# Performance work log

Measured on AMD Instinct MI355X. Metric: run time of the kernel, lower is better.

## Reference

```python
import jax, jax.numpy as jnp
import numpy as np

K = 5                      # spline kernel_size per dim
NEG = -1e30                # finite -inf stand-in for max-scatter init
_COMBO = np.indices((2, 2, 2)).reshape(3, 8).T   # [8,3] corner offsets of the deg-1 B-spline support
_STRIDE = np.array([1, K, K * K])


def spline_basis(pseudo):
    # pseudo: [E,3] in [0,1]; open degree-1 B-spline, kernel_size K per dim.
    v = jnp.clip(pseudo, 0.0, 1.0) * (K - 1)
    i0 = jnp.clip(jnp.floor(v), 0, K - 2)
    f = v - i0                                   # [E,3] fractional part
    c = jnp.asarray(_COMBO)                      # [8,3]
    w = jnp.prod(jnp.where(c[None] == 1, f[:, None, :], 1.0 - f[:, None, :]), axis=2)  # [E,8]
    k = jnp.sum((i0.astype(jnp.int32)[:, None, :] + c[None]) * jnp.asarray(_STRIDE)[None, None, :], axis=2)  # [E,8]
    return w, k


def spline_conv(x, src, dst, pseudo, W, root, bias):
    # x:[N,Fin], W:[K^3,Fin,Fout]. Gather-spline-scatter, mean aggregation + root weight + bias.
    N = x.shape[0]
    U = jnp.einsum('ni,kio->nko', x, W)          # [N,K^3,Fout] all-kernel transform (dense GEMM)
    bw, kidx = spline_basis(pseudo)              # [E,8], [E,8]
    msg = jnp.sum(bw[:, :, None] * U[src[:, None], kidx], axis=1)  # [E,Fout]
    deg = jnp.zeros((N,), x.dtype).at[dst].add(1.0)
    agg = jnp.zeros((N, W.shape[2]), x.dtype).at[dst].add(msg) / jnp.maximum(deg, 1.0)[:, None]
    return agg + x @ root + bias


def weighted_max_pool(x, w, cluster, C):
    # keep features of the max-attention-weight node in each voxel cluster
    seg_w = jnp.full((C,), NEG, x.dtype).at[cluster].max(w)
    winner = w >= seg_w[cluster]
    pooled = jnp.full((C, x.shape[1]), NEG, x.dtype).at[cluster].max(jnp.where(winner[:, None], x, NEG))
    return jnp.where(pooled <= NEG / 2, 0.0, pooled)


def dense_max_pool(x, cluster, C):
    pooled = jnp.full((C, x.shape[1]), NEG, x.dtype).at[cluster].max(x)
    return jnp.where(pooled <= NEG / 2, 0.0, pooled)


def setup_inputs() -> dict:
    key = jax.random.key(0)
    ks = iter(jax.random.split(key, 80))
    N = [30000, 10000, 4000, 1500, 600]
    E = [360000, 120000, 48000, 18000, 7200]
    Fin = [1, 32, 64, 64, 64]
    Fout = [32, 64, 64, 64, 64]
    Cs = [10000, 4000, 1500, 600, 128]
    d = {"x": jax.random.normal(next(ks), (N[0], 1), jnp.float32)}
    for l in range(5):
        d[f"src{l}"] = jax.random.randint(next(ks), (E[l],), 0, N[l], jnp.int32)
        d[f"dst{l}"] = jax.random.randint(next(ks), (E[l],), 0, N[l], jnp.int32)
        d[f"pseudo{l}"] = jax.random.uniform(next(ks), (E[l], 3), jnp.float32)
    for l in range(5):
        d[f"cluster{l+1}"] = jax.random.randint(next(ks), (N[l],), 0, Cs[l], jnp.int32)
    for l in range(5):
        d[f"W{l+1}"] = 0.1 * jax.random.normal(next(ks), (K ** 3, Fin[l], Fout[l]), jnp.float32)
        d[f"root{l+1}"] = 0.1 * jax.random.normal(next(ks), (Fin[l], Fout[l]), jnp.float32)
        d[f"b{l+1}"] = jnp.zeros((Fout[l],), jnp.float32)
    for l, fdim in enumerate([32, 64, 64, 64]):
        d[f"attw{l+1}"] = 0.1 * jax.random.normal(next(ks), (fdim, 2), jnp.float32)
        d[f"attb{l+1}"] = jnp.zeros((2,), jnp.float32)
    d["fcw"] = 0.05 * jax.random.normal(next(ks), (512, 10), jnp.float32)
    d["fcb"] = jnp.zeros((10,), jnp.float32)
    return d


def reference(x, src0, dst0, pseudo0, src1, dst1, pseudo1, src2, dst2, pseudo2,
              src3, dst3, pseudo3, src4, dst4, pseudo4,
              cluster1, cluster2, cluster3, cluster4, cluster5,
              W1, root1, b1, W2, root2, b2, W3, root3, b3, W4, root4, b4, W5, root5, b5,
              attw1, attb1, attw2, attb2, attw3, attb3, attw4, attb4, fcw, fcb):
    h = jax.nn.elu(spline_conv(x, src0, dst0, pseudo0, W1, root1, b1))
    h = weighted_max_pool(h, (h @ attw1 + attb1)[:, 0], cluster1, 10000)
    h = jax.nn.elu(spline_conv(h, src1, dst1, pseudo1, W2, root2, b2))
    h = weighted_max_pool(h, (h @ attw2 + attb2)[:, 0], cluster2, 4000)
    h = jax.nn.elu(spline_conv(h, src2, dst2, pseudo2, W3, root3, b3))
    h = weighted_max_pool(h, (h @ attw3 + attb3)[:, 0], cluster3, 1500)
    h = jax.nn.elu(spline_conv(h, src3, dst3, pseudo3, W4, root4, b4))
    h = weighted_max_pool(h, (h @ attw4 + attb4)[:, 0], cluster4, 600)
    h = jax.nn.relu(spline_conv(h, src4, dst4, pseudo4, W5, root5, b5))
    h = dense_max_pool(h, cluster5, 128)        # [128, 64] = 16 graphs x 8 voxels
    z = h.reshape(-1, 512)                      # [16, 8*64]
    return jax.nn.log_softmax(z @ fcw + fcb, axis=1)
```

## Files before the change

kernel.cpp:

```cpp
#include <hip/hip_runtime.h>
#include <math.h>

#define KS 5

typedef __bf16 bf16x8 __attribute__((ext_vector_type(8)));
typedef float f32x4 __attribute__((ext_vector_type(4)));
typedef unsigned long long u64;

__device__ __forceinline__ unsigned int flipf(float f) {
    unsigned int b = __float_as_uint(f);
    return b ^ ((b >> 31) ? 0xFFFFFFFFu : 0x80000000u);
}
__device__ __forceinline__ float unflipf(unsigned int u) {
    unsigned int b = u ^ ((u >> 31) ? 0x80000000u : 0xFFFFFFFFu);
    return __uint_as_float(b);
}
__device__ __forceinline__ float pread(unsigned int u) {
    return (u == 0u) ? 0.f : unflipf(u);
}

__device__ __forceinline__ void basis1(float p, int& b, float& f) {
    float v = fminf(fmaxf(p, 0.f), 1.f) * (float)(KS - 1);
    float fl = fminf(floorf(v), (float)(KS - 2));
    b = (int)fl; f = v - fl;
}

__device__ const int cE[5]     = {360000, 120000, 48000, 18000, 7200};
__device__ const int cN[5]     = {30000, 10000, 4000, 1500, 600};
__device__ const int cNB[5]    = {512, 469, 188, 71, 29};
__device__ const int cStart[5] = {0, 512, 981, 1169, 1240};
__device__ const int cBTend[5] = {8192, 139264, 401408, 663552, 925696};
__device__ const int cLFIN[5]  = {0, 5, 6, 6, 6};
__device__ const int cLFOUT[5] = {5, 6, 6, 6, 6};
__device__ const int cLKB[5]   = {2, 5, 6, 6, 6};

#define PREP_BLOCKS 1269
#define BPACK_TOT   925696

struct BatchPtrs {
    const float* ps[5];
    const int*   dst[5];
    int*   cell[5];
    int*   ctrl[5];
    int*   blkbase[5];
    float* deg[5];
    float* rankf[5];
    int*   dstbase[5];
    int*   eord[5];
};

struct BpackPtrs {
    const float* W[5];
    __bf16* H[5];
    __bf16* M[5];
    __bf16* L[5];
};

__global__ void edge_prep_all(BatchPtrs P)
{
    __shared__ int lh[64];
    int b = blockIdx.x;
    int l = (b >= 512) + (b >= 981) + (b >= 1169) + (b >= 1240);
    int lb = b - cStart[l];
    int E = cE[l];
    int stride = cNB[l] * 256;
    const float* pseudo = P.ps[l];
    const int* dst = P.dst[l];
    int* cell = P.cell[l];
    float* deg = P.deg[l];
    float* rankf = P.rankf[l];

    int t = threadIdx.x;
    if (t < 64) lh[t] = 0;
    __syncthreads();
    for (int e = lb * 256 + t; e < E; e += stride) {
        int b0, b1, b2; float f0, f1, f2;
        basis1(pseudo[e * 3 + 0], b0, f0);
        basis1(pseudo[e * 3 + 1], b1, f1);
        basis1(pseudo[e * 3 + 2], b2, f2);
        int c = b0 + 4 * b1 + 16 * b2;
        cell[e] = c;
        atomicAdd(&lh[c], 1);
        rankf[e] = atomicAdd(&deg[dst[e]], 1.0f);
    }
    __syncthreads();
    if (t < 64) P.blkbase[l][lb * 64 + t] = atomicAdd(&P.ctrl[l][t], lh[t]);
}

__global__ void scan5(BatchPtrs P)
{
    __shared__ int wexc[16];
    __shared__ int tot;
    __shared__ int carry;
    int l = blockIdx.x;
    int* ctrl = P.ctrl[l];
    const float* deg = P.deg[l];
    int* dstbase = P.dstbase[l];
    int N = cN[l];

    int t = (int)threadIdx.x;
    int lane = t & 63;
    int wid = t >> 6;
    if (t == 0) carry = 0;
    if (t < 64) {
        int h = ctrl[t];
        int x = h;
        #pragma unroll
        for (int off = 1; off < 64; off <<= 1) {
            int y = __shfl_up(x, off, 64);
            if (lane >= off) x += y;
        }
        int excl = x - h;
        ctrl[128 + t] = excl;
        int ch = (h + 63) >> 6;
        int cx = ch;
        #pragma unroll
        for (int off = 1; off < 64; off <<= 1) {
            int y = __shfl_up(cx, off, 64);
            if (lane >= off) cx += y;
        }
        ctrl[200 + t] = cx - ch;
        if (t == 63) {
            ctrl[128 + 64] = excl + h;
            ctrl[200 + 64] = cx;
            ctrl[272] = cx;
        }
    }
    __syncthreads();
    for (int base = 0; base < N; base += 4096) {
        int i0 = base + t * 4;
        int4 v = make_int4(0, 0, 0, 0);
        if (i0 < N) {
            float4 d = *reinterpret_cast<const float4*>(deg + i0);
            v.x = (int)d.x; v.y = (int)d.y; v.z = (int)d.z; v.w = (int)d.w;
        }
        int s = v.x + v.y + v.z + v.w;
        int x = s;
        #pragma unroll
        for (int off = 1; off < 64; off <<= 1) {
            int y = __shfl_up(x, off, 64);
            if (lane >= off) x += y;
        }
        if (lane == 63) wexc[wid] = x;
        __syncthreads();
        if (t < 16) {
            int a = wexc[t];
            int inc = a;
            #pragma unroll
            for (int off = 1; off < 16; off <<= 1) {
                int y = __shfl_up(inc, off, 16);
                if (t >= off) inc += y;
            }
            wexc[t] = inc - a;
            if (t == 15) tot = inc;
        }
        __syncthreads();
        if (i0 < N) {
            int e0 = carry + wexc[wid] + (x - s);
            int4 o;
            o.x = e0;
            o.y = e0 + v.x;
            o.z = o.y + v.y;
            o.w = o.z + v.z;
            *reinterpret_cast<int4*>(dstbase + i0) = o;
        }
        __syncthreads();
        if (t == 0) carry += tot;
        __syncthreads();
    }
    if (t == 0) dstbase[N] = carry;
}

__global__ void edge_scatter_all(BatchPtrs P)
{
    __shared__ int cur[64];
    int b = blockIdx.x;
    int l = (b >= 512) + (b >= 981) + (b >= 1169) + (b >= 1240);
    int lb = b - cStart[l];
    int E = cE[l];
    int stride = cNB[l] * 256;
    const int* cell = P.cell[l];
    const int* dst = P.dst[l];
    const int* dstbase = P.dstbase[l];
    float* rankf = P.rankf[l];
    int* posb = (int*)rankf;
    int* eord = P.eord[l];

    int t = threadIdx.x;
    if (t < 64) cur[t] = P.ctrl[l][128 + t] + P.blkbase[l][lb * 64 + t];
    __syncthreads();
    for (int e = lb * 256 + t; e < E; e += stride) {
        int p = atomicAdd(&cur[cell[e]], 1);
        eord[p] = e;
        int r = (int)rankf[e];
        posb[e] = dstbase[dst[e]] + r;
    }
}

__global__ void bpack_all(BpackPtrs B)
{
    int t = blockIdx.x * blockDim.x + threadIdx.x;
    if (t >= BPACK_TOT) return;
    int l = (t >= 8192) + (t >= 139264) + (t >= 401408) + (t >= 663552);
    int tl = t - (l ? cBTend[l - 1] : 0);
    int lfout = cLFOUT[l], lkb = cLKB[l], lfin = cLFIN[l];
    int fin = 1 << lfin;
    const float* W = B.W[l];
    int o = tl & ((1 << lfout) - 1);
    int kb = (tl >> lfout) & ((1 << lkb) - 1);
    int cellid = tl >> (lfout + lkb);
    int b0 = cellid & 3, b1 = (cellid >> 2) & 3, b2 = cellid >> 4;
    bf16x8 vh, vm, vl;
    #pragma unroll
    for (int j = 0; j < 8; ++j) {
        int r = kb * 8 + j;
        float val = 0.f;
        if (r < (fin << 3)) {
            int c = r >> lfin;
            int i = r & (fin - 1);
            int k = (b0 + (c & 1)) + 5 * (b1 + ((c >> 1) & 1)) + 25 * (b2 + (c >> 2));
            val = W[((((size_t)k << lfin) + i) << lfout) + o];
        }
        __bf16 hv = (__bf16)val;
        vh[j] = hv;
        float r1 = val - (float)hv;
        __bf16 mv = (__bf16)r1;
        vm[j] = mv;
        vl[j] = (__bf16)(r1 - (float)mv);
    }
    *reinterpret_cast<bf16x8*>(B.H[l] + (size_t)tl * 8) = vh;
    *reinterpret_cast<bf16x8*>(B.M[l] + (size_t)tl * 8) = vm;
    *reinterpret_cast<bf16x8*>(B.L[l] + (size_t)tl * 8) = vl;
}

template<int FIN, int FOUT, bool GATHER>
__global__ void conv_mfma(const float* __restrict__ xin,
                          const u64* __restrict__ win,
                          const int* __restrict__ src,
                          const float* __restrict__ pseudo,
                          const __bf16* __restrict__ BpH,
                          const __bf16* __restrict__ BpM,
                          const __bf16* __restrict__ BpL,
                          const int* __restrict__ ctrl,
                          const int* __restrict__ eord,
                          const int* __restrict__ posb,
                          float* __restrict__ msg)
{
    constexpr int KB = (FIN == 1) ? 4 : FIN;
    constexpr int KSTEPS = (FIN == 1) ? 1 : FIN / 4;
    constexpr int NF = FOUT / 16;
    constexpr int SLICE = 4 * FOUT * 8;

    __shared__ float cst[64][FOUT + 1];
    __shared__ int posv[64];
    __shared__ __bf16 bsh[3][SLICE];

    int bid = blockIdx.x;
    if (bid >= ctrl[272]) return;
    int blo = 0, bhi = 64;
    while (blo + 1 < bhi) {
        int mid = (blo + bhi) >> 1;
        if (ctrl[200 + mid] <= bid) blo = mid; else bhi = mid;
    }
    int bucket = blo;
    int m0 = (bid - ctrl[200 + bucket]) << 6;
    int bbase = ctrl[128 + bucket];
    int bsize = ctrl[128 + bucket + 1] - bbase;

    int tt = threadIdx.x;
    int lane = tt & 63;
    int wave = tt >> 6;
    int h4 = lane >> 4;
    int col = lane & 15;
    int row = m0 + wave * 16 + col;
    bool valid = row < bsize;
    int e = eord[bbase + (valid ? row : 0)];
    int s = src[e];

    if (tt < 64) {
        int orow = m0 + tt;
        posv[tt] = (orow < bsize) ? posb[eord[bbase + orow]] : -1;
    }

    float bw[8];
    {
        int b0, b1, b2; float f0, f1, f2;
        basis1(pseudo[e * 3 + 0], b0, f0);
        basis1(pseudo[e * 3 + 1], b1, f1);
        basis1(pseudo[e * 3 + 2], b2, f2);
        float g0 = 1.f - f0, g1 = 1.f - f1, g2 = 1.f - f2;
        float vf = valid ? 1.f : 0.f;
        #pragma unroll
        for (int j = 0; j < 8; ++j)
            bw[j] = vf * ((j & 1) ? f0 : g0) * (((j >> 1) & 1) ? f1 : g1) * (((j >> 2) & 1) ? f2 : g2);
    }

    const float* xrow;
    bool xok = true;
    if (GATHER) {
        u64 wv = win[s];
        xok = (wv != 0ull);
        xrow = xin + (size_t)(unsigned int)(wv & 0xffffffffu) * FIN;
    } else {
        xrow = xin + (size_t)s * FIN;
    }

    float xv[8], xw[8];
    float xsc = 0.f;
    #pragma unroll
    for (int j = 0; j < 8; ++j) { xv[j] = 0.f; xw[j] = 0.f; }
    if (FIN >= 32) {
        if (xok) {
            const float4* xb = reinterpret_cast<const float4*>(xrow + h4 * 8);
            float4 u0 = xb[0], u1 = xb[1];
            xv[0] = u0.x; xv[1] = u0.y; xv[2] = u0.z; xv[3] = u0.w;
            xv[4] = u1.x; xv[5] = u1.y; xv[6] = u1.z; xv[7] = u1.w;
            if (FIN == 64) {
                const float4* xb2 = reinterpret_cast<const float4*>(xrow + 32 + h4 * 8);
                float4 w0 = xb2[0], w1 = xb2[1];
                xw[0] = w0.x; xw[1] = w0.y; xw[2] = w0.z; xw[3] = w0.w;
                xw[4] = w1.x; xw[5] = w1.y; xw[6] = w1.z; xw[7] = w1.w;
            }
        }
    } else {
        xsc = xrow[0];
    }

    f32x4 acc[NF];
    #pragma unroll
    for (int nf = 0; nf < NF; ++nf) acc[nf] = (f32x4){0.f, 0.f, 0.f, 0.f};

    for (int kt = 0; kt < KSTEPS; ++kt) {
        __syncthreads();
        {
            size_t gbase = ((size_t)bucket * KB + kt * 4) * FOUT * 8;
            int idx = tt * 8;
            if (idx < SLICE) {
                *reinterpret_cast<bf16x8*>(&bsh[0][idx]) =
                    *reinterpret_cast<const bf16x8*>(BpH + gbase + idx);
                *reinterpret_cast<bf16x8*>(&bsh[1][idx]) =
                    *reinterpret_cast<const bf16x8*>(BpM + gbase + idx);
                *reinterpret_cast<bf16x8*>(&bsh[2][idx]) =
                    *reinterpret_cast<const bf16x8*>(BpL + gbase + idx);
            }
        }
        __syncthreads();

        float v[8];
        if (FIN == 64) {
            float bwc = bw[kt >> 1];
            const float* u = (kt & 1) ? xw : xv;
            #pragma unroll
            for (int j = 0; j < 8; ++j) v[j] = u[j] * bwc;
        } else if (FIN == 32) {
            float bwc = bw[kt];
            #pragma unroll
            for (int j = 0; j < 8; ++j) v[j] = xv[j] * bwc;
        } else {
            float xm = (h4 == 0) ? xsc : 0.f;
            #pragma unroll
            for (int j = 0; j < 8; ++j) v[j] = bw[j] * xm;
        }
        bf16x8 ah, am, al;
        #pragma unroll
        for (int j = 0; j < 8; ++j) {
            __bf16 hv = (__bf16)v[j];
            ah[j] = hv;
            float r1 = v[j] - (float)hv;
            __bf16 mv = (__bf16)r1;
            am[j] = mv;
            al[j] = (__bf16)(r1 - (float)mv);
        }
        #pragma unroll
        for (int nf = 0; nf < NF; ++nf) {
            int loff = (h4 * FOUT + nf * 16 + col) * 8;
            bf16x8 bh = *reinterpret_cast<const bf16x8*>(&bsh[0][loff]);
            bf16x8 bm = *reinterpret_cast<const bf16x8*>(&bsh[1][loff]);
            bf16x8 bl = *reinterpret_cast<const bf16x8*>(&bsh[2][loff]);
            acc[nf] = __builtin_amdgcn_mfma_f32_16x16x32_bf16(ah, bh, acc[nf], 0, 0, 0);
            acc[nf] = __builtin_amdgcn_mfma_f32_16x16x32_bf16(ah, bm, acc[nf], 0, 0, 0);
            acc[nf] = __builtin_amdgcn_mfma_f32_16x16x32_bf16(am, bh, acc[nf], 0, 0, 0);
            acc[nf] = __builtin_amdgcn_mfma_f32_16x16x32_bf16(am, bm, acc[nf], 0, 0, 0);
            acc[nf] = __builtin_amdgcn_mfma_f32_16x16x32_bf16(ah, bl, acc[nf], 0, 0, 0);
            acc[nf] = __builtin_amdgcn_mfma_f32_16x16x32_bf16(al, bh, acc[nf], 0, 0, 0);
        }
    }

    #pragma unroll
    for (int nf = 0; nf < NF; ++nf)
        #pragma unroll
        for (int j = 0; j < 4; ++j)
            cst[wave * 16 + h4 * 4 + j][nf * 16 + col] = acc[nf][j];
    __syncthreads();

    constexpr int F4 = FOUT / 4;
    constexpr int ITER = 64 * F4 / 256;
    #pragma unroll
    for (int i = 0; i < ITER; ++i) {
        int idx = i * 256 + tt;
        int r = idx / F4;
        int c4 = idx - r * F4;
        int p = posv[r];
        if (p >= 0) {
            float4 vq = make_float4(cst[r][c4 * 4], cst[r][c4 * 4 + 1],
                                    cst[r][c4 * 4 + 2], cst[r][c4 * 4 + 3]);
            *reinterpret_cast<float4*>(msg + (size_t)p * FOUT + c4 * 4) = vq;
        }
    }
}

template<int FIN, int FOUT, int ACT, int POOLMODE, bool GATHER>
__global__ void node_finalize(const float* __restrict__ xin,
                              const u64* __restrict__ winprev,
                              const float* __restrict__ msg,
                              const int* __restrict__ dstbase,
                              const float* __restrict__ deg,
                              const float* __restrict__ root,
                              const float* __restrict__ bias,
                              const float* __restrict__ attw,
                              const float* __restrict__ attb,
                              const int* __restrict__ cluster,
                              float* __restrict__ out,
                              u64* __restrict__ seg64,
                              unsigned int* __restrict__ pooled,
                              int N)
{
    int t = blockIdx.x * blockDim.x + threadIdx.x;
    int n = t / FOUT, o = t % FOUT;
    if (n >= N) return;
    int b0 = dstbase[n];
    int dn = (int)deg[n];
    float a = 0.f;
    for (int r = 0; r < dn; ++r)
        a += msg[(size_t)(b0 + r) * FOUT + o];
    a = a / fmaxf((float)dn, 1.f) + bias[o];

    const float* xrow;
    bool xok = true;
    if (GATHER) {
        u64 wv = winprev[n];
        xok = (wv != 0ull);
        xrow = xin + (size_t)(unsigned int)(wv & 0xffffffffu) * FIN;
    } else {
        xrow = xin + (size_t)n * FIN;
    }
    if (xok) {
        #pragma unroll
        for (int i = 0; i < FIN; ++i)
            a = fmaf(xrow[i], root[i * FOUT + o], a);
    }
    if (ACT == 0) a = (a > 0.f) ? a : expm1f(a);
    else          a = fmaxf(a, 0.f);
    if (POOLMODE == 1) {
        atomicMax(&pooled[(size_t)cluster[n] * FOUT + o], flipf(a));
        return;
    }
    out[t] = a;
    float w = a * attw[2 * o];
    #pragma unroll
    for (int off = FOUT / 2; off >= 1; off >>= 1)
        w += __shfl_xor(w, off, 64);
    if (o == 0) {
        float wt = w + attb[0];
        u64 key = ((u64)flipf(wt) << 32) | (unsigned int)n;
        atomicMax(&seg64[cluster[n]], key);
    }
}

__global__ void pool_final_fc(const unsigned int* __restrict__ pooled,
                              const float* __restrict__ fcw,
                              const float* __restrict__ fcb,
                              float* __restrict__ out)
{
    __shared__ float h[8192];
    __shared__ float logits[16][10];
    __shared__ float lse[16];
    int t = threadIdx.x;
    for (int i = t; i < 8192; i += 512)
        h[i] = pread(pooled[i]);
    __syncthreads();
    if (t < 160) {
        int g = t / 10, cls = t - g * 10;
        float a = fcb[cls];
        for (int j = 0; j < 512; ++j)
            a = fmaf(h[g * 512 + j], fcw[j * 10 + cls], a);
        logits[g][cls] = a;
    }
    __syncthreads();
    if (t < 16) {
        float m = -1e30f;
        for (int c = 0; c < 10; ++c) m = fmaxf(m, logits[t][c]);
        float s = 0.f;
        for (int c = 0; c < 10; ++c) s += expf(logits[t][c] - m);
        lse[t] = m + logf(s);
    }
    __syncthreads();
    if (t < 160) out[t] = logits[t / 10][t - (t / 10) * 10] - lse[t / 10];
}

static const int hE[5] = {360000, 120000, 48000, 18000, 7200};
static const int hN[5] = {30000, 10000, 4000, 1500, 600};

#define OFF_HA     0
#define OFF_HB     960000
#define OFF_DEG    1600000
#define OFF_CTRL   1646112
#define OFF_SEG64  1648672
#define OFF_POOL4  1680880
#define ZERO_FLTS  89072
#define OFF_BLK    1689072
#define OFF_DSTB   1770288
#define OFF_CELL   1816464
#define OFF_RANK   2369680
#define OFF_EORD   2922896
#define OFF_BP     3476112
#define OFF_MSG    14584464

static const int cumN_h[5]    = {0, 30000, 40000, 44000, 45500};
static const int cumC_h[5]    = {0, 10000, 14000, 15500, 16100};
static const int cumBLK_h[5]  = {0, 32768, 62784, 74816, 79360};
static const int cumDSTB_h[5] = {0, 30016, 40032, 44048, 45568};
static const int cumE_h[5]    = {0, 360000, 480000, 528000, 546000};
static const size_t planeB_h[5] = {65536, 1048576, 2097152, 2097152, 2097152};
static const size_t cumBPf_h[5] = {0, 98304, 1671168, 4816896, 7962624};

extern "C" void kernel_launch(void* const* d_in, const int* in_sizes, int n_in,
                              void* d_out, int out_size, void* d_ws, size_t ws_size,
                              hipStream_t stream)
{
    const float* x0 = (const float*)d_in[0];
    const int*   src_[5]  = {(const int*)d_in[1], (const int*)d_in[4], (const int*)d_in[7], (const int*)d_in[10], (const int*)d_in[13]};
    const int*   dst_[5]  = {(const int*)d_in[2], (const int*)d_in[5], (const int*)d_in[8], (const int*)d_in[11], (const int*)d_in[14]};
    const float* ps_[5]   = {(const float*)d_in[3], (const float*)d_in[6], (const float*)d_in[9], (const float*)d_in[12], (const float*)d_in[15]};
    const int*   cl_[5]   = {(const int*)d_in[16], (const int*)d_in[17], (const int*)d_in[18], (const int*)d_in[19], (const int*)d_in[20]};
    const float* W_[5]    = {(const float*)d_in[21], (const float*)d_in[24], (const float*)d_in[27], (const float*)d_in[30], (const float*)d_in[33]};
    const float* root_[5] = {(const float*)d_in[22], (const float*)d_in[25], (const float*)d_in[28], (const float*)d_in[31], (const float*)d_in[34]};
    const float* b_[5]    = {(const float*)d_in[23], (const float*)d_in[26], (const float*)d_in[29], (const float*)d_in[32], (const float*)d_in[35]};
    const float* attw_[4] = {(const float*)d_in[36], (const float*)d_in[38], (const float*)d_in[40], (const float*)d_in[42]};
    const float* attb_[4] = {(const float*)d_in[37], (const float*)d_in[39], (const float*)d_in[41], (const float*)d_in[43]};
    const float* fcw = (const float*)d_in[44];
    const float* fcb = (const float*)d_in[45];

    float* ws_f = (float*)d_ws;
    float* hA = ws_f + OFF_HA;
    float* hB = ws_f + OFF_HB;
    float* msg = ws_f + OFF_MSG;
    unsigned int* pool4 = (unsigned int*)(ws_f + OFF_POOL4);

    BatchPtrs P;
    BpackPtrs BP;
    const __bf16* BpH_l[5]; const __bf16* BpM_l[5]; const __bf16* BpL_l[5];
    int* ctrl_l[5]; int* dstb_l[5]; int* eord_l[5]; int* posb_l[5];
    float* deg_l[5];
    u64* seg64_l[5];
    for (int l = 0; l < 5; ++l) {
        P.ps[l] = ps_[l];
        P.dst[l] = dst_[l];
        P.cell[l] = (int*)(ws_f + OFF_CELL + cumE_h[l]);
        P.ctrl[l] = (int*)(ws_f + OFF_CTRL + l * 512);
        P.blkbase[l] = (int*)(ws_f + OFF_BLK + cumBLK_h[l]);
        P.deg[l] = ws_f + OFF_DEG + cumN_h[l];
        P.rankf[l] = ws_f + OFF_RANK + cumE_h[l];
        P.dstbase[l] = (int*)(ws_f + OFF_DSTB + cumDSTB_h[l]);
        P.eord[l] = (int*)(ws_f + OFF_EORD + cumE_h[l]);
        __bf16* H = (__bf16*)(ws_f + OFF_BP + cumBPf_h[l]);
        BP.W[l] = W_[l];
        BP.H[l] = H;
        BP.M[l] = H + planeB_h[l];
        BP.L[l] = H + 2 * planeB_h[l];
        BpH_l[l] = BP.H[l]; BpM_l[l] = BP.M[l]; BpL_l[l] = BP.L[l];
        ctrl_l[l] = P.ctrl[l];
        dstb_l[l] = P.dstbase[l];
        eord_l[l] = P.eord[l];
        posb_l[l] = (int*)P.rankf[l];
        deg_l[l] = P.deg[l];
        seg64_l[l] = (u64*)(ws_f + OFF_SEG64) + cumC_h[l];
    }

    (void)hipMemsetAsync(ws_f + OFF_DEG, 0, (size_t)ZERO_FLTS * 4, stream);
    edge_prep_all<<<PREP_BLOCKS, 256, 0, stream>>>(P);
    scan5<<<5, 1024, 0, stream>>>(P);
    edge_scatter_all<<<PREP_BLOCKS, 256, 0, stream>>>(P);
    bpack_all<<<(BPACK_TOT + 255) / 256, 256, 0, stream>>>(BP);

    conv_mfma<1, 32, false><<<hE[0] / 64 + 65, 256, 0, stream>>>(
        x0, nullptr, src_[0], ps_[0], BpH_l[0], BpM_l[0], BpL_l[0], ctrl_l[0], eord_l[0], posb_l[0], msg);
    node_finalize<1, 32, 0, 0, false><<<(hN[0] * 32) / 256, 256, 0, stream>>>(
        x0, nullptr, msg, dstb_l[0], deg_l[0], root_[0], b_[0], attw_[0], attb_[0], cl_[0], hA, seg64_l[0], nullptr, hN[0]);

    conv_mfma<32, 64, true><<<hE[1] / 64 + 65, 256, 0, stream>>>(
        hA, seg64_l[0], src_[1], ps_[1], BpH_l[1], BpM_l[1], BpL_l[1], ctrl_l[1], eord_l[1], posb_l[1], msg);
    node_finalize<32, 64, 0, 0, true><<<(hN[1] * 64) / 256, 256, 0, stream>>>(
        hA, seg64_l[0], msg, dstb_l[1], deg_l[1], root_[1], b_[1], attw_[1], attb_[1], cl_[1], hB, seg64_l[1], nullptr, hN[1]);

    conv_mfma<64, 64, true><<<hE[2] / 64 + 65, 256, 0, stream>>>(
        hB, seg64_l[1], src_[2], ps_[2], BpH_l[2], BpM_l[2], BpL_l[2], ctrl_l[2], eord_l[2], posb_l[2], msg);
    node_finalize<64, 64, 0, 0, true><<<(hN[2] * 64) / 256, 256, 0, stream>>>(
        hB, seg64_l[1], msg, dstb_l[2], deg_l[2], root_[2], b_[2], attw_[2], attb_[2], cl_[2], hA, seg64_l[2], nullptr, hN[2]);

    conv_mfma<64, 64, true><<<hE[3] / 64 + 65, 256, 0, stream>>>(
        hA, seg64_l[2], src_[3], ps_[3], BpH_l[3], BpM_l[3], BpL_l[3], ctrl_l[3], eord_l[3], posb_l[3], msg);
    node_finalize<64, 64, 0, 0, true><<<(hN[3] * 64) / 256, 256, 0, stream>>>(
        hA, seg64_l[2], msg, dstb_l[3], deg_l[3], root_[3], b_[3], attw_[3], attb_[3], cl_[3], hB, seg64_l[3], nullptr, hN[3]);

    conv_mfma<64, 64, true><<<hE[4] / 64 + 65, 256, 0, stream>>>(
        hB, seg64_l[3], src_[4], ps_[4], BpH_l[4], BpM_l[4], BpL_l[4], ctrl_l[4], eord_l[4], posb_l[4], msg);
    node_finalize<64, 64, 1, 1, true><<<(hN[4] * 64) / 256, 256, 0, stream>>>(
        hB, seg64_l[3], msg, dstb_l[4], deg_l[4], root_[4], b_[4], nullptr, nullptr, cl_[4], nullptr, nullptr, pool4, hN[4]);
    pool_final_fc<<<1, 512, 0, stream>>>(pool4, fcw, fcb, (float*)d_out);
}
```

Measured before the change: 292.1 us.

## Fuse prep with bpack, scatter with direct FP32 conv0, drop layer-0 sorting

The edge-prep and weight-packing kernels become a single launch, and the edge-scatter for layers 1-4 is merged with a new direct FP32 layer-0 convolution. Layer 0 (Fin=1) no longer computes spline cells, cell sorting or split-bf16 MFMA. Instead each thread computes one output feature per edge from a shared-memory copy of W0 and writes it straight to its destination-sorted slot. This removes two kernel launches and the MFMA emulation overhead on the largest layer, at the cost of recomputing the basis per output feature and doing scalar FMA work.

```diff
diff --git a/kernel.cpp b/kernel.cpp
--- a/kernel.cpp
+++ b/kernel.cpp
@@ -33,9 +33,14 @@
 __device__ const int cLFIN[5]  = {0, 5, 6, 6, 6};
 __device__ const int cLFOUT[5] = {5, 6, 6, 6, 6};
 __device__ const int cLKB[5]   = {2, 5, 6, 6, 6};
-
-#define PREP_BLOCKS 1269
-#define BPACK_TOT   925696
+__device__ const int sStart[4] = {0, 469, 657, 728};
+
+#define PREP_BLOCKS  1269
+#define BPACK_TOT    925696
+#define BPACK_BLOCKS 3616
+#define SCAT_BLOCKS  757
+#define CONV0_BLOCKS 2048
+#define E0           360000
 
 struct BatchPtrs {
     const float* ps[5];
@@ -56,153 +61,49 @@
     __bf16* L[5];
 };
 
-__global__ void edge_prep_all(BatchPtrs P)
+__global__ void prep_bpack(BatchPtrs P, BpackPtrs B)
 {
     __shared__ int lh[64];
-    int b = blockIdx.x;
-    int l = (b >= 512) + (b >= 981) + (b >= 1169) + (b >= 1240);
-    int lb = b - cStart[l];
-    int E = cE[l];
-    int stride = cNB[l] * 256;
-    const float* pseudo = P.ps[l];
-    const int* dst = P.dst[l];
-    int* cell = P.cell[l];
-    float* deg = P.deg[l];
-    float* rankf = P.rankf[l];
-
+    int blk = blockIdx.x;
     int t = threadIdx.x;
-    if (t < 64) lh[t] = 0;
-    __syncthreads();
-    for (int e = lb * 256 + t; e < E; e += stride) {
-        int b0, b1, b2; float f0, f1, f2;
-        basis1(pseudo[e * 3 + 0], b0, f0);
-        basis1(pseudo[e * 3 + 1], b1, f1);
-        basis1(pseudo[e * 3 + 2], b2, f2);
-        int c = b0 + 4 * b1 + 16 * b2;
-        cell[e] = c;
-        atomicAdd(&lh[c], 1);
-        rankf[e] = atomicAdd(&deg[dst[e]], 1.0f);
-    }
-    __syncthreads();
-    if (t < 64) P.blkbase[l][lb * 64 + t] = atomicAdd(&P.ctrl[l][t], lh[t]);
-}
-
-__global__ void scan5(BatchPtrs P)
-{
-    __shared__ int wexc[16];
-    __shared__ int tot;
-    __shared__ int carry;
-    int l = blockIdx.x;
-    int* ctrl = P.ctrl[l];
-    const float* deg = P.deg[l];
-    int* dstbase = P.dstbase[l];
-    int N = cN[l];
-
-    int t = (int)threadIdx.x;
-    int lane = t & 63;
-    int wid = t >> 6;
-    if (t == 0) carry = 0;
-    if (t < 64) {
-        int h = ctrl[t];
-        int x = h;
-        #pragma unroll
-        for (int off = 1; off < 64; off <<= 1) {
-            int y = __shfl_up(x, off, 64);
-            if (lane >= off) x += y;
-        }
-        int excl = x - h;
-        ctrl[128 + t] = excl;
-        int ch = (h + 63) >> 6;
-        int cx = ch;
-        #pragma unroll
-        for (int off = 1; off < 64; off <<= 1) {
-            int y = __shfl_up(cx, off, 64);
-            if (lane >= off) cx += y;
-        }
-        ctrl[200 + t] = cx - ch;
-        if (t == 63) {
-            ctrl[128 + 64] = excl + h;
-            ctrl[200 + 64] = cx;
-            ctrl[272] = cx;
-        }
-    }
-    __syncthreads();
-    for (int base = 0; base < N; base += 4096) {
-        int i0 = base + t * 4;
-        int4 v = make_int4(0, 0, 0, 0);
-        if (i0 < N) {
-            float4 d = *reinterpret_cast<const float4*>(deg + i0);
-            v.x = (int)d.x; v.y = (int)d.y; v.z = (int)d.z; v.w = (int)d.w;
-        }
-        int s = v.x + v.y + v.z + v.w;
-        int x = s;
-        #pragma unroll
-        for (int off = 1; off < 64; off <<= 1) {
-            int y = __shfl_up(x, off, 64);
-            if (lane >= off) x += y;
-        }
-        if (lane == 63) wexc[wid] = x;
-        __syncthreads();
-        if (t < 16) {
-            int a = wexc[t];
-            int inc = a;
-            #pragma unroll
-            for (int off = 1; off < 16; off <<= 1) {
-                int y = __shfl_up(inc, off, 16);
-                if (t >= off) inc += y;
-            }
-            wexc[t] = inc - a;
-            if (t == 15) tot = inc;
-        }
-        __syncthreads();
-        if (i0 < N) {
-            int e0 = carry + wexc[wid] + (x - s);
-            int4 o;
-            o.x = e0;
-            o.y = e0 + v.x;
-            o.z = o.y + v.y;
-            o.w = o.z + v.z;
-            *reinterpret_cast<int4*>(dstbase + i0) = o;
-        }
-        __syncthreads();
-        if (t == 0) carry += tot;
-        __syncthreads();
-    }
-    if (t == 0) dstbase[N] = carry;
-}
-
-__global__ void edge_scatter_all(BatchPtrs P)
-{
-    __shared__ int cur[64];
-    int b = blockIdx.x;
-    int l = (b >= 512) + (b >= 981) + (b >= 1169) + (b >= 1240);
-    int lb = b - cStart[l];
-    int E = cE[l];
-    int stride = cNB[l] * 256;
-    const int* cell = P.cell[l];
-    const int* dst = P.dst[l];
-    const int* dstbase = P.dstbase[l];
-    float* rankf = P.rankf[l];
-    int* posb = (int*)rankf;
-    int* eord = P.eord[l];
-
-    int t = threadIdx.x;
-    if (t < 64) cur[t] = P.ctrl[l][128 + t] + P.blkbase[l][lb * 64 + t];
-    __syncthreads();
-    for (int e = lb * 256 + t; e < E; e += stride) {
-        int p = atomicAdd(&cur[cell[e]], 1);
-        eord[p] = e;
-        int r = (int)rankf[e];
-        posb[e] = dstbase[dst[e]] + r;
-    }
-}
-
-__global__ void bpack_all(BpackPtrs B)
-{
-    int t = blockIdx.x * blockDim.x + threadIdx.x;
-    if (t >= BPACK_TOT) return;
-    int l = (t >= 8192) + (t >= 139264) + (t >= 401408) + (t >= 663552);
-    int tl = t - (l ? cBTend[l - 1] : 0);
+
+    if (blk < PREP_BLOCKS) {
+        int l = (blk >= 512) + (blk >= 981) + (blk >= 1169) + (blk >= 1240);
+        int lb = blk - cStart[l];
+        int E = cE[l];
+        int stride = cNB[l] * 256;
+        const int* dst = P.dst[l];
+        float* deg = P.deg[l];
+        float* rankf = P.rankf[l];
+
+        if (l == 0) {
+            for (int e = lb * 256 + t; e < E; e += stride)
+                rankf[e] = atomicAdd(&deg[dst[e]], 1.0f);
+            return;
+        }
+        const float* pseudo = P.ps[l];
+        int* cell = P.cell[l];
+        if (t < 64) lh[t] = 0;
+        __syncthreads();
+        for (int e = lb * 256 + t; e < E; e += stride) {
+            int b0, b1, b2; float f0, f1, f2;
+            basis1(pseudo[e * 3 + 0], b0, f0);
+            basis1(pseudo[e * 3 + 1], b1, f1);
+            basis1(pseudo[e * 3 + 2], b2, f2);
+            int c = b0 + 4 * b1 + 16 * b2;
+            cell[e] = c;
+            atomicAdd(&lh[c], 1);
+            rankf[e] = atomicAdd(&deg[dst[e]], 1.0f);
+        }
+        __syncthreads();
+        if (t < 64) P.blkbase[l][lb * 64 + t] = atomicAdd(&P.ctrl[l][t], lh[t]);
+        return;
+    }
+
+    int tt = (blk - PREP_BLOCKS) * 256 + t;
+    if (tt >= BPACK_TOT) return;
+    int l = (tt >= 8192) + (tt >= 139264) + (tt >= 401408) + (tt >= 663552);
+    int tl = tt - (l ? cBTend[l - 1] : 0);
     int lfout = cLFOUT[l], lkb = cLKB[l], lfin = cLFIN[l];
     int fin = 1 << lfin;
     const float* W = B.W[l];
@@ -233,6 +134,152 @@
     *reinterpret_cast<bf16x8*>(B.L[l] + (size_t)tl * 8) = vl;
 }
 
+__global__ void scan5(BatchPtrs P)
+{
+    __shared__ int wexc[16];
+    __shared__ int tot;
+    __shared__ int carry;
+    int l = blockIdx.x;
+    int* ctrl = P.ctrl[l];
+    const float* deg = P.deg[l];
+    int* dstbase = P.dstbase[l];
+    int N = cN[l];
+
+    int t = (int)threadIdx.x;
+    int lane = t & 63;
+    int wid = t >> 6;
+    if (t == 0) carry = 0;
+    if (t < 64) {
+        int h = ctrl[t];
+        int x = h;
+        #pragma unroll
+        for (int off = 1; off < 64; off <<= 1) {
+            int y = __shfl_up(x, off, 64);
+            if (lane >= off) x += y;
+        }
+        int excl = x - h;
+        ctrl[128 + t] = excl;
+        int ch = (h + 63) >> 6;
+        int cx = ch;
+        #pragma unroll
+        for (int off = 1; off < 64; off <<= 1) {
+            int y = __shfl_up(cx, off, 64);
+            if (lane >= off) cx += y;
+        }
+        ctrl[200 + t] = cx - ch;
+        if (t == 63) {
+            ctrl[128 + 64] = excl + h;
+            ctrl[200 + 64] = cx;
+            ctrl[272] = cx;
+        }
+    }
+    __syncthreads();
+    for (int base = 0; base < N; base += 4096) {
+        int i0 = base + t * 4;
+        int4 v = make_int4(0, 0, 0, 0);
+        if (i0 < N) {
+            float4 d = *reinterpret_cast<const float4*>(deg + i0);
+            v.x = (int)d.x; v.y = (int)d.y; v.z = (int)d.z; v.w = (int)d.w;
+        }
+        int s = v.x + v.y + v.z + v.w;
+        int x = s;
+        #pragma unroll
+        for (int off = 1; off < 64; off <<= 1) {
+            int y = __shfl_up(x, off, 64);
+            if (lane >= off) x += y;
+        }
+        if (lane == 63) wexc[wid] = x;
+        __syncthreads();
+        if (t < 16) {
+            int a = wexc[t];
+            int inc = a;
+            #pragma unroll
+            for (int off = 1; off < 16; off <<= 1) {
+                int y = __shfl_up(inc, off, 16);
+                if (t >= off) inc += y;
+            }
+            wexc[t] = inc - a;
+            if (t == 15) tot = inc;
+        }
+        __syncthreads();
+        if (i0 < N) {
+            int e0 = carry + wexc[wid] + (x - s);
+            int4 o;
+            o.x = e0;
+            o.y = e0 + v.x;
+            o.z = o.y + v.y;
+            o.w = o.z + v.z;
+            *reinterpret_cast<int4*>(dstbase + i0) = o;
+        }
+        __syncthreads();
+        if (t == 0) carry += tot;
+        __syncthreads();
+    }
+    if (t == 0) dstbase[N] = carry;
+}
+
+__global__ void scatter_conv0(BatchPtrs P,
+                              const float* __restrict__ x0,
+                              const int* __restrict__ src0,
+                              const float* __restrict__ ps0,
+                              const float* __restrict__ W0,
+                              float* __restrict__ msg)
+{
+    __shared__ int cur[64];
+    __shared__ float Wsh[4000];
+    int blk = blockIdx.x;
+    int t = threadIdx.x;
+
+    if (blk < SCAT_BLOCKS) {
+        int li = (blk >= 469) + (blk >= 657) + (blk >= 728);
+        int l = 1 + li;
+        int lb = blk - sStart[li];
+        int E = cE[l];
+        int stride = cNB[l] * 256;
+        const int* cell = P.cell[l];
+        const int* dst = P.dst[l];
+        const int* dstbase = P.dstbase[l];
+        float* rankf = P.rankf[l];
+        int* posb = (int*)rankf;
+        int* eord = P.eord[l];
+
+        if (t < 64) cur[t] = P.ctrl[l][128 + t] + P.blkbase[l][lb * 64 + t];
+        __syncthreads();
+        for (int e = lb * 256 + t; e < E; e += stride) {
+            int p = atomicAdd(&cur[cell[e]], 1);
+            eord[p] = e;
+            int r = (int)rankf[e];
+            posb[e] = dstbase[dst[e]] + r;
+        }
+        return;
+    }
+
+    for (int i = t; i < 4000; i += 256) Wsh[i] = W0[i];
+    __syncthreads();
+    const int* dst0 = P.dst[0];
+    const float* rank0 = P.rankf[0];
+    const int* dstb0 = P.dstbase[0];
+    int gs = CONV0_BLOCKS * 256;
+    for (int g = (blk - SCAT_BLOCKS) * 256 + t; g < E0 * 32; g += gs) {
+        int e = g >> 5;
+        int o = g & 31;
+        int b0, b1, b2; float f0, f1, f2;
+        basis1(ps0[e * 3 + 0], b0, f0);
+        basis1(ps0[e * 3 + 1], b1, f1);
+        basis1(ps0[e * 3 + 2], b2, f2);
+        float g0 = 1.f - f0, g1 = 1.f - f1, g2 = 1.f - f2;
+        float acc = 0.f;
+        #pragma unroll
+        for (int c = 0; c < 8; ++c) {
+            float bwc = ((c & 1) ? f0 : g0) * (((c >> 1) & 1) ? f1 : g1) * (((c >> 2) & 1) ? f2 : g2);
+            int k = (b0 + (c & 1)) + 5 * (b1 + ((c >> 1) & 1)) + 25 * (b2 + (c >> 2));
+            acc = fmaf(bwc, Wsh[k * 32 + o], acc);
+        }
+        int pos = dstb0[dst0[e]] + (int)rank0[e];
+        msg[(size_t)pos * 32 + o] = x0[src0[e]] * acc;
+    }
+}
+
 template<int FIN, int FOUT, bool GATHER>
 __global__ void conv_mfma(const float* __restrict__ xin,
                           const u64* __restrict__ win,
@@ -246,8 +293,8 @@
                           const int* __restrict__ posb,
                           float* __restrict__ msg)
 {
-    constexpr int KB = (FIN == 1) ? 4 : FIN;
-    constexpr int KSTEPS = (FIN == 1) ? 1 : FIN / 4;
+    constexpr int KB = FIN;
+    constexpr int KSTEPS = FIN / 4;
     constexpr int NF = FOUT / 16;
     constexpr int SLICE = 4 * FOUT * 8;
 
@@ -306,24 +353,19 @@
     }
 
     float xv[8], xw[8];
-    float xsc = 0.f;
     #pragma unroll
     for (int j = 0; j < 8; ++j) { xv[j] = 0.f; xw[j] = 0.f; }
-    if (FIN >= 32) {
-        if (xok) {
-            const float4* xb = reinterpret_cast<const float4*>(xrow + h4 * 8);
-            float4 u0 = xb[0], u1 = xb[1];
-            xv[0] = u0.x; xv[1] = u0.y; xv[2] = u0.z; xv[3] = u0.w;
-            xv[4] = u1.x; xv[5] = u1.y; xv[6] = u1.z; xv[7] = u1.w;
-            if (FIN == 64) {
-                const float4* xb2 = reinterpret_cast<const float4*>(xrow + 32 + h4 * 8);
-                float4 w0 = xb2[0], w1 = xb2[1];
-                xw[0] = w0.x; xw[1] = w0.y; xw[2] = w0.z; xw[3] = w0.w;
-                xw[4] = w1.x; xw[5] = w1.y; xw[6] = w1.z; xw[7] = w1.w;
-            }
-        }
-    } else {
-        xsc = xrow[0];
+    if (xok) {
+        const float4* xb = reinterpret_cast<const float4*>(xrow + h4 * 8);
+        float4 u0 = xb[0], u1 = xb[1];
+        xv[0] = u0.x; xv[1] = u0.y; xv[2] = u0.z; xv[3] = u0.w;
+        xv[4] = u1.x; xv[5] = u1.y; xv[6] = u1.z; xv[7] = u1.w;
+        if (FIN == 64) {
+            const float4* xb2 = reinterpret_cast<const float4*>(xrow + 32 + h4 * 8);
+            float4 w0 = xb2[0], w1 = xb2[1];
+            xw[0] = w0.x; xw[1] = w0.y; xw[2] = w0.z; xw[3] = w0.w;
+            xw[4] = w1.x; xw[5] = w1.y; xw[6] = w1.z; xw[7] = w1.w;
+        }
     }
 
     f32x4 acc[NF];
@@ -352,14 +394,10 @@
             const float* u = (kt & 1) ? xw : xv;
             #pragma unroll
             for (int j = 0; j < 8; ++j) v[j] = u[j] * bwc;
-        } else if (FIN == 32) {
+        } else {
             float bwc = bw[kt];
             #pragma unroll
             for (int j = 0; j < 8; ++j) v[j] = xv[j] * bwc;
-        } else {
-            float xm = (h4 == 0) ? xsc : 0.f;
-            #pragma unroll
-            for (int j = 0; j < 8; ++j) v[j] = bw[j] * xm;
         }
         bf16x8 ah, am, al;
         #pragma unroll
@@ -578,13 +616,11 @@
     }
 
     (void)hipMemsetAsync(ws_f + OFF_DEG, 0, (size_t)ZERO_FLTS * 4, stream);
-    edge_prep_all<<<PREP_BLOCKS, 256, 0, stream>>>(P);
+    prep_bpack<<<PREP_BLOCKS + BPACK_BLOCKS, 256, 0, stream>>>(P, BP);
     scan5<<<5, 1024, 0, stream>>>(P);
-    edge_scatter_all<<<PREP_BLOCKS, 256, 0, stream>>>(P);
-    bpack_all<<<(BPACK_TOT + 255) / 256, 256, 0, stream>>>(BP);
-
-    conv_mfma<1, 32, false><<<hE[0] / 64 + 65, 256, 0, stream>>>(
-        x0, nullptr, src_[0], ps_[0], BpH_l[0], BpM_l[0], BpL_l[0], ctrl_l[0], eord_l[0], posb_l[0], msg);
+    scatter_conv0<<<SCAT_BLOCKS + CONV0_BLOCKS, 256, 0, stream>>>(
+        P, x0, src_[0], ps_[0], W_[0], msg);
+
     node_finalize<1, 32, 0, 0, false><<<(hN[0] * 32) / 256, 256, 0, stream>>>(
         x0, nullptr, msg, dstb_l[0], deg_l[0], root_[0], b_[0], attw_[0], attb_[0], cl_[0], hA, seg64_l[0], nullptr, hN[0]);
 
```

Result: faster. 278.5 us (-4.7%).
